# Performance work log

Measured on AMD Instinct MI355X. Metric: run time of the kernel, lower is better.

## Reference

```python
import jax, jax.numpy as jnp
import numpy as np

B, H, W, C = 4, 64, 64, 256
D = C // 8  # q/k projection dim


def setup_inputs() -> dict:
    key = jax.random.key(0)
    ks = jax.random.split(key, 5)
    scale = lambda fan_in: 1.0 / np.sqrt(fan_in)
    return {
        "x": jax.random.normal(ks[0], (B, H, W, C), dtype=jnp.float32),
        "wq": jax.random.normal(ks[1], (C, D), dtype=jnp.float32) * scale(C),
        "bq": jnp.zeros((D,), dtype=jnp.float32),
        "wk": jax.random.normal(ks[2], (C, D), dtype=jnp.float32) * scale(C),
        "bk": jnp.zeros((D,), dtype=jnp.float32),
        "wv": jax.random.normal(ks[3], (C, C), dtype=jnp.float32) * scale(C),
        "bv": jnp.zeros((C,), dtype=jnp.float32),
        "wo": jax.random.normal(ks[4], (C, C), dtype=jnp.float32) * scale(C),
        "bo": jnp.zeros((C,), dtype=jnp.float32),
    }


def reference(x, wq, bq, wk, bk, wv, bv, wo, bo):
    b, h, w, c = x.shape
    n = h * w
    xt = x.reshape(b, n, c)  # 1x1 conv == per-pixel linear over channels
    q = xt @ wq + bq                      # [b, n, d]
    k = xt @ wk + bk                      # [b, n, d]
    v = xt @ wv + bv                      # [b, n, c]
    scores = jnp.einsum("bnd,bmd->bnm", q, k) / jnp.sqrt(jnp.float32(k.shape[-1]))
    attn = jax.nn.softmax(scores, axis=-1)  # [b, n, n]
    attended = jnp.einsum("bnm,bmc->bnc", attn, v)  # [b, n, c]
    out = attended @ wo + bo
    return x + out.reshape(b, h, w, c)
```

## Files before the change

kernel.cpp:

```cpp
#include <hip/hip_runtime.h>
#include <math.h>

#define B_   4
#define N_   4096
#define C_   256
#define D_   32

typedef __attribute__((ext_vector_type(8))) short short8;
typedef __attribute__((ext_vector_type(4))) float f32x4;
typedef __attribute__((ext_vector_type(4))) unsigned short us4;

__device__ __forceinline__ unsigned short f2bf(float f) {
    unsigned int u = __float_as_uint(f);
    u = (u + 0x7FFFu + ((u >> 16) & 1u)) >> 16;
    return (unsigned short)u;
}
__device__ __forceinline__ unsigned short p2bf(float f) {
    return (unsigned short)((__float_as_uint(f) + 0x8000u) >> 16);
}
__device__ __forceinline__ float bf2f(unsigned short h) {
    return __uint_as_float(((unsigned int)h) << 16);
}

__device__ __forceinline__ void dma16(const unsigned short* g, unsigned short* l) {
    __builtin_amdgcn_global_load_lds(
        (const __attribute__((address_space(1))) unsigned int*)(uintptr_t)(g),
        (__attribute__((address_space(3))) unsigned int*)(unsigned int)(uintptr_t)(l),
        16, 0, 0);
}

__global__ __launch_bounds__(256) void prep_w_kernel(const float* __restrict__ wq,
                                                     const float* __restrict__ wk,
                                                     const float* __restrict__ wv,
                                                     const float* __restrict__ wo,
                                                     unsigned short* __restrict__ wqkvT,
                                                     unsigned short* __restrict__ woT) {
    int idx = blockIdx.x * 256 + threadIdx.x;
    if (idx < 320 * 256) {
        int n = idx >> 8, c = idx & 255;
        float v = (n < 32) ? wq[c * 32 + n]
                : (n < 64) ? wk[c * 32 + (n - 32)]
                           : wv[c * 256 + (n - 64)];
        wqkvT[idx] = f2bf(v);
    } else {
        int j = idx - 320 * 256;
        int n = j >> 8, c = j & 255;
        woT[j] = f2bf(wo[c * 256 + n]);
    }
}

__global__ __launch_bounds__(256) void qkv_gemm_kernel(const float* __restrict__ x,
        const unsigned short* __restrict__ wqkvT,
        const float* __restrict__ bq, const float* __restrict__ bk, const float* __restrict__ bv,
        unsigned short* __restrict__ qb, unsigned short* __restrict__ kb,
        unsigned short* __restrict__ vT) {
    const int tid = threadIdx.x;
    const int wave = tid >> 6, lane = tid & 63;
    const int quad = lane >> 4, li = lane & 15;
    const int rows0 = blockIdx.x * 32;
    const int bb = rows0 >> 12, ni0 = rows0 & 4095;
    const float kS = 0.17677669529663687f * 1.4426950408889634f;

    __shared__ __align__(16) unsigned short sbuf[10240];

#pragma unroll
    for (int i = 0; i < 8; ++i) {
        int flat = i * 256 + tid;
        int row = flat >> 6, c4 = flat & 63;
        float4 f = *(const float4*)(x + (size_t)(rows0 + row) * 256 + c4 * 4);
        us4 o = { f2bf(f.x), f2bf(f.y), f2bf(f.z), f2bf(f.w) };
        *(us4*)&sbuf[row * 264 + c4 * 4] = o;
    }
    __syncthreads();

    const int rowt = wave & 1;
    const int nt0 = (wave >> 1) * 10;
    const int r0 = rows0 + rowt * 16;

    short8 A[8];
#pragma unroll
    for (int kc = 0; kc < 8; ++kc)
        A[kc] = *(const short8*)&sbuf[(rowt * 16 + li) * 264 + kc * 32 + quad * 8];
    __syncthreads();

#pragma unroll
    for (int j = 0; j < 10; ++j) {
        const int nt = nt0 + j;
        f32x4 acc = {0.f, 0.f, 0.f, 0.f};
#pragma unroll
        for (int kc = 0; kc < 8; ++kc) {
            short8 Bf = *(const short8*)(wqkvT + (size_t)(nt * 16 + li) * 256 + kc * 32 + quad * 8);
            acc = __builtin_amdgcn_mfma_f32_16x16x32_bf16(A[kc], Bf, acc, 0, 0, 0);
        }
        int n = nt * 16 + li;
        float bias = (nt < 2) ? bq[n] : (nt < 4) ? bk[n - 32] : bv[n - 64];
        if (nt < 4) {
            unsigned short* dst = (nt < 2) ? qb : kb;
            float scl = (nt < 2) ? kS : 1.0f;
            int d = (nt < 2) ? n : (n - 32);
#pragma unroll
            for (int jj = 0; jj < 4; ++jj)
                dst[(size_t)(r0 + quad * 4 + jj) * 32 + d] = f2bf((acc[jj] + bias) * scl);
        } else {
            int c = n - 64;
            int lp = rowt * 16 + quad * 4;
            us4 hv = { f2bf(acc[0] + bias), f2bf(acc[1] + bias),
                       f2bf(acc[2] + bias), f2bf(acc[3] + bias) };
            *(us4*)&sbuf[c * 40 + lp] = hv;
        }
    }
    __syncthreads();

    {
        const unsigned short* src = sbuf + tid * 40;
        unsigned short* dstv = vT + ((size_t)(bb * 256 + tid) * 4096 + ni0);
#pragma unroll
        for (int k2 = 0; k2 < 4; ++k2)
            *(short8*)(dstv + k2 * 8) = *(const short8*)(src + k2 * 8);
    }
}

__global__ __launch_bounds__(256, 2) void attn_partial_kernel(
        const unsigned short* __restrict__ qb, const unsigned short* __restrict__ kb,
        const unsigned short* __restrict__ vT,
        unsigned short* __restrict__ Obf, float* __restrict__ ml) {
    const int tid = threadIdx.x;
    const int wave = tid >> 6, lane = tid & 63;
    const int quad = lane >> 4, li = lane & 15;

    const int bid = blockIdx.x;
    const int xcd = bid & 7, jj_ = bid >> 3;
    const int qt = jj_ & 31;
    const int g = (xcd << 1) | (jj_ >> 5);
    const int by = g >> 2, sg = g & 3;
    const int pw = qt * 128 + wave * 32;
    const int key0 = sg * 1024;

    __shared__ __align__(16) unsigned short smem[21504];
    unsigned short* v0 = smem;
    unsigned short* v1 = smem + 8192;
    unsigned short* pw_ = smem + 16384 + wave * 1280;

    short8 a_q[2];
#pragma unroll
    for (int qf = 0; qf < 2; ++qf)
        a_q[qf] = *(const short8*)(qb + (size_t)(by * N_ + pw + qf * 16 + li) * 32 + quad * 8);

    const int o8 = lane >> 3, s8 = lane & 7;
    const int sp = s8 ^ o8;
    const int chl = sp >> 2, chk = sp & 3;
    auto stage = [&](int kt, unsigned short* buf) {
#pragma unroll
        for (int h = 0; h < 4; ++h) {
            int ch = ((h * 32 + wave * 8 + o8) << 1) + chl;
            const unsigned short* g2 = vT + (size_t)(by * 256 + ch) * 4096
                                         + key0 + kt * 32 + chk * 8;
            dma16(g2, buf + (h * 256 + wave * 64) * 8);
        }
    };

    stage(0, v0);

    const f32x4 Z = {0.f, 0.f, 0.f, 0.f};
    f32x4 O[2][16];
#pragma unroll
    for (int qf = 0; qf < 2; ++qf)
#pragma unroll
        for (int ct = 0; ct < 16; ++ct) O[qf][ct] = Z;
    f32x4 lsum[2] = {Z, Z};
    short8 ones;
#pragma unroll
    for (int j = 0; j < 8; ++j) ones[j] = (short)0x3F80;

    short8 kf0, kf1;
    {
        const unsigned short* krow = kb + (size_t)(by * N_ + key0) * 32;
        kf0 = *(const short8*)(krow + li * 32 + quad * 8);
        kf1 = *(const short8*)(krow + (16 + li) * 32 + quad * 8);
    }

    const int voff = (li >> 1) * 64 + ((((li & 1) * 4 + quad) ^ ((li >> 1) & 7)) * 8);

    unsigned short* vc = v0;
    unsigned short* vn = v1;
#pragma unroll 1
    for (int kt = 0; kt < 32; ++kt) {
        __builtin_amdgcn_s_waitcnt(0x0f70);
        __syncthreads();

        short8 kn0 = kf0, kn1 = kf1;
        if (kt < 31) {
            stage(kt + 1, vn);
            const unsigned short* krow = kb + (size_t)(by * N_ + key0 + (kt + 1) * 32) * 32;
            kn0 = *(const short8*)(krow + li * 32 + quad * 8);
            kn1 = *(const short8*)(krow + (16 + li) * 32 + quad * 8);
        }

#pragma unroll
        for (int qf = 0; qf < 2; ++qf) {
            f32x4 s0 = __builtin_amdgcn_mfma_f32_16x16x32_bf16(a_q[qf], kf0, Z, 0, 0, 0);
            f32x4 s1 = __builtin_amdgcn_mfma_f32_16x16x32_bf16(a_q[qf], kf1, Z, 0, 0, 0);
#pragma unroll
            for (int r = 0; r < 4; ++r) {
                float p0 = __builtin_amdgcn_exp2f(s0[r]);
                float p1 = __builtin_amdgcn_exp2f(s1[r]);
                pw_[(qf * 16 + quad * 4 + r) * 40 + li]      = p2bf(p0);
                pw_[(qf * 16 + quad * 4 + r) * 40 + 16 + li] = p2bf(p1);
            }
        }

        short8 ap0 = *(const short8*)(pw_ + li * 40 + quad * 8);
        short8 ap1 = *(const short8*)(pw_ + (16 + li) * 40 + quad * 8);
        lsum[0] = __builtin_amdgcn_mfma_f32_16x16x32_bf16(ap0, ones, lsum[0], 0, 0, 0);
        lsum[1] = __builtin_amdgcn_mfma_f32_16x16x32_bf16(ap1, ones, lsum[1], 0, 0, 0);
#pragma unroll
        for (int ct = 0; ct < 16; ++ct) {
            short8 bv8 = *(const short8*)(vc + ct * 512 + voff);
            O[0][ct] = __builtin_amdgcn_mfma_f32_16x16x32_bf16(ap0, bv8, O[0][ct], 0, 0, 0);
            O[1][ct] = __builtin_amdgcn_mfma_f32_16x16x32_bf16(ap1, bv8, O[1][ct], 0, 0, 0);
        }

        kf0 = kn0; kf1 = kn1;
        unsigned short* t = vc; vc = vn; vn = t;
    }

    __syncthreads();
    unsigned short* att = smem + wave * 4224;
    const int srow = lane & 15, scc = (lane >> 4) * 64;
#pragma unroll
    for (int qf = 0; qf < 2; ++qf) {
#pragma unroll
        for (int ct = 0; ct < 16; ++ct)
#pragma unroll
            for (int r = 0; r < 4; ++r)
                att[(quad * 4 + r) * 264 + ct * 16 + li] = f2bf(O[qf][ct][r]);
        const int pbase = by * N_ + pw + qf * 16;
        unsigned short* dst = Obf + ((size_t)(pbase + srow) * 4 + sg) * 256 + scc;
#pragma unroll
        for (int h = 0; h < 8; ++h)
            *(short8*)(dst + h * 8) = *(const short8*)(att + srow * 264 + scc + h * 8);
        if (li == 0) {
#pragma unroll
            for (int r = 0; r < 4; ++r) {
                int pp = pbase + quad * 4 + r;
                ml[pp * 4 + sg] = lsum[qf][r];
            }
        }
    }
}

__global__ __launch_bounds__(256) void merge_proj_kernel(
        const unsigned short* __restrict__ Obf, const float* __restrict__ ml,
        const unsigned short* __restrict__ woT, const float* __restrict__ x,
        const float* __restrict__ bo, float* __restrict__ out) {
    const int tid = threadIdx.x;
    const int px = blockIdx.x * 16;
    __shared__ __align__(16) unsigned short att[16 * 264];

    {
        const int row = tid >> 4, chc = tid & 15;
        const int p = px + row;
        float lt = ml[p * 4] + ml[p * 4 + 1] + ml[p * 4 + 2] + ml[p * 4 + 3];
        float inv = 1.0f / lt;
        float acc[16];
#pragma unroll
        for (int i = 0; i < 16; ++i) acc[i] = 0.f;
#pragma unroll
        for (int s = 0; s < 4; ++s) {
            const unsigned short* src = Obf + (size_t)(p * 4 + s) * 256 + chc * 16;
            short8 v0 = *(const short8*)(src);
            short8 v1 = *(const short8*)(src + 8);
#pragma unroll
            for (int jj = 0; jj < 8; ++jj) {
                acc[jj]     += bf2f((unsigned short)v0[jj]);
                acc[8 + jj] += bf2f((unsigned short)v1[jj]);
            }
        }
        short8 o0, o1;
#pragma unroll
        for (int jj = 0; jj < 8; ++jj) {
            o0[jj] = (short)f2bf(acc[jj] * inv);
            o1[jj] = (short)f2bf(acc[8 + jj] * inv);
        }
        *(short8*)&att[row * 264 + chc * 16]     = o0;
        *(short8*)&att[row * 264 + chc * 16 + 8] = o1;
    }
    __syncthreads();

    const int wave = tid >> 6, lane = tid & 63;
    const int quad = lane >> 4, li = lane & 15;
    short8 bfr[8];
#pragma unroll
    for (int kc = 0; kc < 8; ++kc)
        bfr[kc] = *(const short8*)&att[li * 264 + kc * 32 + quad * 8];
#pragma unroll
    for (int mt = 0; mt < 4; ++mt) {
        const int mtg = wave * 4 + mt;
        f32x4 acc = {0.f, 0.f, 0.f, 0.f};
#pragma unroll
        for (int kc = 0; kc < 8; ++kc) {
            short8 aw = *(const short8*)(woT + (size_t)(mtg * 16 + li) * 256 + kc * 32 + quad * 8);
            acc = __builtin_amdgcn_mfma_f32_16x16x32_bf16(aw, bfr[kc], acc, 0, 0, 0);
        }
        const int pg = px + li;
        const float4 xv  = *(const float4*)(x  + (size_t)pg * 256 + mtg * 16 + quad * 4);
        const float4 bv4 = *(const float4*)(bo + mtg * 16 + quad * 4);
        float4 o4;
        o4.x = acc[0] + xv.x + bv4.x;
        o4.y = acc[1] + xv.y + bv4.y;
        o4.z = acc[2] + xv.z + bv4.z;
        o4.w = acc[3] + xv.w + bv4.w;
        *(float4*)(out + (size_t)pg * 256 + mtg * 16 + quad * 4) = o4;
    }
}

extern "C" void kernel_launch(void* const* d_in, const int* in_sizes, int n_in,
                              void* d_out, int out_size, void* d_ws, size_t ws_size,
                              hipStream_t stream) {
    const float* x  = (const float*)d_in[0];
    const float* wq = (const float*)d_in[1];
    const float* bq = (const float*)d_in[2];
    const float* wk = (const float*)d_in[3];
    const float* bk = (const float*)d_in[4];
    const float* wv = (const float*)d_in[5];
    const float* bv = (const float*)d_in[6];
    const float* wo = (const float*)d_in[7];
    const float* bo = (const float*)d_in[8];
    float* out = (float*)d_out;

    char* ws = (char*)d_ws;
    unsigned short* wqkvT = (unsigned short*)(ws);
    unsigned short* woT   = (unsigned short*)(ws +   163840);
    unsigned short* qb    = (unsigned short*)(ws +   294912);
    unsigned short* kb    = (unsigned short*)(ws +  1343488);
    unsigned short* vT    = (unsigned short*)(ws +  2392064);
    unsigned short* Obf   = (unsigned short*)(ws + 10780672);
    float*          ml    = (float*)         (ws + 44335104);

    hipLaunchKernelGGL(prep_w_kernel,      dim3(576),  dim3(256), 0, stream, wq, wk, wv, wo, wqkvT, woT);
    hipLaunchKernelGGL(qkv_gemm_kernel,    dim3(512),  dim3(256), 0, stream, x, wqkvT, bq, bk, bv, qb, kb, vT);
    hipLaunchKernelGGL(attn_partial_kernel,dim3(512),  dim3(256), 0, stream, qb, kb, vT, Obf, ml);
    hipLaunchKernelGGL(merge_proj_kernel,  dim3(1024), dim3(256), 0, stream, Obf, ml, woT, x, bo, out);
}
```

Baseline: 176.3 us.

## Fuse four stage kernels into one cooperative kernel with grid syncs

```diff
diff --git a/kernel.cpp b/kernel.cpp
--- a/kernel.cpp
+++ b/kernel.cpp
@@ -1,5 +1,8 @@
 #include <hip/hip_runtime.h>
+#include <hip/hip_cooperative_groups.h>
 #include <math.h>
+
+namespace cg = cooperative_groups;
 
 #define B_   4
 #define N_   4096
@@ -28,6 +31,7 @@
         (__attribute__((address_space(3))) unsigned int*)(unsigned int)(uintptr_t)(l),
         16, 0, 0);
 }
+
 
 __global__ __launch_bounds__(256) void prep_w_kernel(const float* __restrict__ wq,
                                                      const float* __restrict__ wk,
@@ -314,6 +318,282 @@
     }
 }
 
+__global__ __launch_bounds__(256, 2) void fused_kernel(
+        const float* __restrict__ x,
+        const float* __restrict__ wq, const float* __restrict__ bq,
+        const float* __restrict__ wk, const float* __restrict__ bk,
+        const float* __restrict__ wv, const float* __restrict__ bv,
+        const float* __restrict__ wo, const float* __restrict__ bo,
+        unsigned short* __restrict__ wqkvT, unsigned short* __restrict__ woT,
+        unsigned short* __restrict__ qb, unsigned short* __restrict__ kb,
+        unsigned short* __restrict__ vT,
+        unsigned short* __restrict__ Obf, float* __restrict__ ml,
+        float* __restrict__ out) {
+    cg::grid_group grid = cg::this_grid();
+    const int tid = threadIdx.x;
+    const int wave = tid >> 6, lane = tid & 63;
+    const int quad = lane >> 4, li = lane & 15;
+    const int bidx = blockIdx.x;
+
+    __shared__ __align__(16) unsigned short smem[21504];
+
+    for (int idx = bidx * 256 + tid; idx < 147456; idx += 131072) {
+        if (idx < 81920) {
+            int n = idx >> 8, c = idx & 255;
+            float v = (n < 32) ? wq[c * 32 + n]
+                    : (n < 64) ? wk[c * 32 + (n - 32)]
+                               : wv[c * 256 + (n - 64)];
+            wqkvT[idx] = f2bf(v);
+        } else {
+            int j = idx - 81920;
+            int n = j >> 8, c = j & 255;
+            woT[j] = f2bf(wo[c * 256 + n]);
+        }
+    }
+    grid.sync();
+
+    {
+        const int rows0 = bidx * 32;
+        const int bb = rows0 >> 12, ni0 = rows0 & 4095;
+        const float kS = 0.17677669529663687f * 1.4426950408889634f;
+#pragma unroll
+        for (int i = 0; i < 8; ++i) {
+            int flat = i * 256 + tid;
+            int row = flat >> 6, c4 = flat & 63;
+            float4 f = *(const float4*)(x + (size_t)(rows0 + row) * 256 + c4 * 4);
+            us4 o = { f2bf(f.x), f2bf(f.y), f2bf(f.z), f2bf(f.w) };
+            *(us4*)&smem[row * 264 + c4 * 4] = o;
+        }
+        __syncthreads();
+
+        const int rowt = wave & 1;
+        const int nt0 = (wave >> 1) * 10;
+        const int r0 = rows0 + rowt * 16;
+
+        short8 A[8];
+#pragma unroll
+        for (int kc = 0; kc < 8; ++kc)
+            A[kc] = *(const short8*)&smem[(rowt * 16 + li) * 264 + kc * 32 + quad * 8];
+        __syncthreads();
+
+#pragma unroll
+        for (int j = 0; j < 10; ++j) {
+            const int nt = nt0 + j;
+            f32x4 acc = {0.f, 0.f, 0.f, 0.f};
+#pragma unroll
+            for (int kc = 0; kc < 8; ++kc) {
+                short8 Bf = *(const short8*)(wqkvT + (size_t)(nt * 16 + li) * 256 + kc * 32 + quad * 8);
+                acc = __builtin_amdgcn_mfma_f32_16x16x32_bf16(A[kc], Bf, acc, 0, 0, 0);
+            }
+            int n = nt * 16 + li;
+            float bias = (nt < 2) ? bq[n] : (nt < 4) ? bk[n - 32] : bv[n - 64];
+            if (nt < 4) {
+                unsigned short* dst = (nt < 2) ? qb : kb;
+                float scl = (nt < 2) ? kS : 1.0f;
+                int d = (nt < 2) ? n : (n - 32);
+#pragma unroll
+                for (int jj = 0; jj < 4; ++jj)
+                    dst[(size_t)(r0 + quad * 4 + jj) * 32 + d] = f2bf((acc[jj] + bias) * scl);
+            } else {
+                int c = n - 64;
+                int lp = rowt * 16 + quad * 4;
+                us4 hv = { f2bf(acc[0] + bias), f2bf(acc[1] + bias),
+                           f2bf(acc[2] + bias), f2bf(acc[3] + bias) };
+                *(us4*)&smem[c * 40 + lp] = hv;
+            }
+        }
+        __syncthreads();
+        {
+            const unsigned short* src = smem + tid * 40;
+            unsigned short* dstv = vT + ((size_t)(bb * 256 + tid) * 4096 + ni0);
+#pragma unroll
+            for (int k2 = 0; k2 < 4; ++k2)
+                *(short8*)(dstv + k2 * 8) = *(const short8*)(src + k2 * 8);
+        }
+    }
+    grid.sync();
+
+    {
+        const int xcd = bidx & 7, jj_ = bidx >> 3;
+        const int qt = jj_ & 31;
+        const int g = (xcd << 1) | (jj_ >> 5);
+        const int by = g >> 2, sg = g & 3;
+        const int pw = qt * 128 + wave * 32;
+        const int key0 = sg * 1024;
+
+        unsigned short* v0 = smem;
+        unsigned short* v1 = smem + 8192;
+        unsigned short* pw_ = smem + 16384 + wave * 1280;
+
+        short8 a_q[2];
+#pragma unroll
+        for (int qf = 0; qf < 2; ++qf)
+            a_q[qf] = *(const short8*)(qb + (size_t)(by * N_ + pw + qf * 16 + li) * 32 + quad * 8);
+
+        const int o8 = lane >> 3, s8 = lane & 7;
+        const int sp = s8 ^ o8;
+        const int chl = sp >> 2, chk = sp & 3;
+        auto stage = [&](int kt, unsigned short* buf) {
+#pragma unroll
+            for (int h = 0; h < 4; ++h) {
+                int ch = ((h * 32 + wave * 8 + o8) << 1) + chl;
+                const unsigned short* g2 = vT + (size_t)(by * 256 + ch) * 4096
+                                             + key0 + kt * 32 + chk * 8;
+                dma16(g2, buf + (h * 256 + wave * 64) * 8);
+            }
+        };
+
+        stage(0, v0);
+
+        const f32x4 Z = {0.f, 0.f, 0.f, 0.f};
+        f32x4 O[2][16];
+#pragma unroll
+        for (int qf = 0; qf < 2; ++qf)
+#pragma unroll
+            for (int ct = 0; ct < 16; ++ct) O[qf][ct] = Z;
+        f32x4 lsum[2] = {Z, Z};
+        short8 ones;
+#pragma unroll
+        for (int j = 0; j < 8; ++j) ones[j] = (short)0x3F80;
+
+        short8 kf0, kf1;
+        {
+            const unsigned short* krow = kb + (size_t)(by * N_ + key0) * 32;
+            kf0 = *(const short8*)(krow + li * 32 + quad * 8);
+            kf1 = *(const short8*)(krow + (16 + li) * 32 + quad * 8);
+        }
+
+        const int voff = (li >> 1) * 64 + ((((li & 1) * 4 + quad) ^ ((li >> 1) & 7)) * 8);
+
+        unsigned short* vc = v0;
+        unsigned short* vn = v1;
+#pragma unroll 1
+        for (int kt = 0; kt < 32; ++kt) {
+            __builtin_amdgcn_s_waitcnt(0x0f70);
+            __syncthreads();
+
+            short8 kn0 = kf0, kn1 = kf1;
+            if (kt < 31) {
+                stage(kt + 1, vn);
+                const unsigned short* krow = kb + (size_t)(by * N_ + key0 + (kt + 1) * 32) * 32;
+                kn0 = *(const short8*)(krow + li * 32 + quad * 8);
+                kn1 = *(const short8*)(krow + (16 + li) * 32 + quad * 8);
+            }
+
+#pragma unroll
+            for (int qf = 0; qf < 2; ++qf) {
+                f32x4 s0 = __builtin_amdgcn_mfma_f32_16x16x32_bf16(a_q[qf], kf0, Z, 0, 0, 0);
+                f32x4 s1 = __builtin_amdgcn_mfma_f32_16x16x32_bf16(a_q[qf], kf1, Z, 0, 0, 0);
+#pragma unroll
+                for (int r = 0; r < 4; ++r) {
+                    float p0 = __builtin_amdgcn_exp2f(s0[r]);
+                    float p1 = __builtin_amdgcn_exp2f(s1[r]);
+                    pw_[(qf * 16 + quad * 4 + r) * 40 + li]      = p2bf(p0);
+                    pw_[(qf * 16 + quad * 4 + r) * 40 + 16 + li] = p2bf(p1);
+                }
+            }
+
+            short8 ap0 = *(const short8*)(pw_ + li * 40 + quad * 8);
+            short8 ap1 = *(const short8*)(pw_ + (16 + li) * 40 + quad * 8);
+            lsum[0] = __builtin_amdgcn_mfma_f32_16x16x32_bf16(ap0, ones, lsum[0], 0, 0, 0);
+            lsum[1] = __builtin_amdgcn_mfma_f32_16x16x32_bf16(ap1, ones, lsum[1], 0, 0, 0);
+#pragma unroll
+            for (int ct = 0; ct < 16; ++ct) {
+                short8 bv8 = *(const short8*)(vc + ct * 512 + voff);
+                O[0][ct] = __builtin_amdgcn_mfma_f32_16x16x32_bf16(ap0, bv8, O[0][ct], 0, 0, 0);
+                O[1][ct] = __builtin_amdgcn_mfma_f32_16x16x32_bf16(ap1, bv8, O[1][ct], 0, 0, 0);
+            }
+
+            kf0 = kn0; kf1 = kn1;
+            unsigned short* t = vc; vc = vn; vn = t;
+        }
+
+        __syncthreads();
+        unsigned short* att = smem + wave * 4224;
+        const int srow = lane & 15, scc = (lane >> 4) * 64;
+#pragma unroll
+        for (int qf = 0; qf < 2; ++qf) {
+#pragma unroll
+            for (int ct = 0; ct < 16; ++ct)
+#pragma unroll
+                for (int r = 0; r < 4; ++r)
+                    att[(quad * 4 + r) * 264 + ct * 16 + li] = f2bf(O[qf][ct][r]);
+            const int pbase = by * N_ + pw + qf * 16;
+            unsigned short* dst = Obf + ((size_t)(pbase + srow) * 4 + sg) * 256 + scc;
+#pragma unroll
+            for (int h = 0; h < 8; ++h)
+                *(short8*)(dst + h * 8) = *(const short8*)(att + srow * 264 + scc + h * 8);
+            if (li == 0) {
+#pragma unroll
+                for (int r = 0; r < 4; ++r) {
+                    int pp = pbase + quad * 4 + r;
+                    ml[pp * 4 + sg] = lsum[qf][r];
+                }
+            }
+        }
+    }
+    grid.sync();
+
+#pragma unroll 1
+    for (int half = 0; half < 2; ++half) {
+        const int px = bidx * 32 + half * 16;
+        __syncthreads();
+        {
+            const int row = tid >> 4, chc = tid & 15;
+            const int p = px + row;
+            float lt = ml[p * 4] + ml[p * 4 + 1] + ml[p * 4 + 2] + ml[p * 4 + 3];
+            float inv = 1.0f / lt;
+            float acc[16];
+#pragma unroll
+            for (int i = 0; i < 16; ++i) acc[i] = 0.f;
+#pragma unroll
+            for (int s = 0; s < 4; ++s) {
+                const unsigned short* src = Obf + (size_t)(p * 4 + s) * 256 + chc * 16;
+                short8 v0 = *(const short8*)(src);
+                short8 v1 = *(const short8*)(src + 8);
+#pragma unroll
+                for (int jj = 0; jj < 8; ++jj) {
+                    acc[jj]     += bf2f((unsigned short)v0[jj]);
+                    acc[8 + jj] += bf2f((unsigned short)v1[jj]);
+                }
+            }
+            short8 o0, o1;
+#pragma unroll
+            for (int jj = 0; jj < 8; ++jj) {
+                o0[jj] = (short)f2bf(acc[jj] * inv);
+                o1[jj] = (short)f2bf(acc[8 + jj] * inv);
+            }
+            *(short8*)&smem[row * 264 + chc * 16]     = o0;
+            *(short8*)&smem[row * 264 + chc * 16 + 8] = o1;
+        }
+        __syncthreads();
+
+        short8 bfr[8];
+#pragma unroll
+        for (int kc = 0; kc < 8; ++kc)
+            bfr[kc] = *(const short8*)&smem[li * 264 + kc * 32 + quad * 8];
+#pragma unroll
+        for (int mt = 0; mt < 4; ++mt) {
+            const int mtg = wave * 4 + mt;
+            f32x4 acc = {0.f, 0.f, 0.f, 0.f};
+#pragma unroll
+            for (int kc = 0; kc < 8; ++kc) {
+                short8 aw = *(const short8*)(woT + (size_t)(mtg * 16 + li) * 256 + kc * 32 + quad * 8);
+                acc = __builtin_amdgcn_mfma_f32_16x16x32_bf16(aw, bfr[kc], acc, 0, 0, 0);
+            }
+            const int pg = px + li;
+            const float4 xv  = *(const float4*)(x  + (size_t)pg * 256 + mtg * 16 + quad * 4);
+            const float4 bv4 = *(const float4*)(bo + mtg * 16 + quad * 4);
+            float4 o4;
+            o4.x = acc[0] + xv.x + bv4.x;
+            o4.y = acc[1] + xv.y + bv4.y;
+            o4.z = acc[2] + xv.z + bv4.z;
+            o4.w = acc[3] + xv.w + bv4.w;
+            *(float4*)(out + (size_t)pg * 256 + mtg * 16 + quad * 4) = o4;
+        }
+    }
+}
+
 extern "C" void kernel_launch(void* const* d_in, const int* in_sizes, int n_in,
                               void* d_out, int out_size, void* d_ws, size_t ws_size,
                               hipStream_t stream) {
@@ -337,8 +617,20 @@
     unsigned short* Obf   = (unsigned short*)(ws + 10780672);
     float*          ml    = (float*)         (ws + 44335104);
 
-    hipLaunchKernelGGL(prep_w_kernel,      dim3(576),  dim3(256), 0, stream, wq, wk, wv, wo, wqkvT, woT);
-    hipLaunchKernelGGL(qkv_gemm_kernel,    dim3(512),  dim3(256), 0, stream, x, wqkvT, bq, bk, bv, qb, kb, vT);
-    hipLaunchKernelGGL(attn_partial_kernel,dim3(512),  dim3(256), 0, stream, qb, kb, vT, Obf, ml);
-    hipLaunchKernelGGL(merge_proj_kernel,  dim3(1024), dim3(256), 0, stream, Obf, ml, woT, x, bo, out);
-}
+    void* args[] = {
+        (void*)&x, (void*)&wq, (void*)&bq, (void*)&wk, (void*)&bk,
+        (void*)&wv, (void*)&bv, (void*)&wo, (void*)&bo,
+        (void*)&wqkvT, (void*)&woT, (void*)&qb, (void*)&kb, (void*)&vT,
+        (void*)&Obf, (void*)&ml, (void*)&out
+    };
+    hipError_t cerr = hipLaunchCooperativeKernel((const void*)fused_kernel,
+                                                 dim3(512), dim3(256),
+                                                 args, 0, stream);
+    if (cerr != hipSuccess) {
+        (void)hipGetLastError();
+        hipLaunchKernelGGL(prep_w_kernel,      dim3(576),  dim3(256), 0, stream, wq, wk, wv, wo, wqkvT, woT);
+        hipLaunchKernelGGL(qkv_gemm_kernel,    dim3(512),  dim3(256), 0, stream, x, wqkvT, bq, bk, bv, qb, kb, vT);
+        hipLaunchKernelGGL(attn_partial_kernel,dim3(512),  dim3(256), 0, stream, qb, kb, vT, Obf, ml);
+        hipLaunchKernelGGL(merge_proj_kernel,  dim3(1024), dim3(256), 0, stream, Obf, ml, woT, x, bo, out);
+    }
+}
```

New measurement: 400.2 us. +127.0%, slower.
